# Optimization experiments

Hardware: AMD Instinct MI355X
Metric: run time of the kernel (lower is better)

## Reference

```python
import jax, jax.numpy as jnp
import numpy as np

N = 50000          # nodes
E = 800000         # directed edges (before self-loops)
NUM_CLASSES = 10
NEG_SLOPE = 0.2    # PyG GATConv default leaky_relu slope


def segment_softmax(logits, seg, num_segments):
    # numerically stable softmax over edges grouped by target node
    m = jax.ops.segment_max(logits, seg, num_segments=num_segments)
    e = jnp.exp(logits - m[seg])
    s = jax.ops.segment_sum(e, seg, num_segments=num_segments)
    return e / s[seg]


def gat_conv(x, src, dst, W, a_src, a_dst, b, n_nodes):
    # single-head PyG-style GATConv (eval mode: attention dropout disabled)
    h = x @ W                              # [N, C]
    alpha_src = h @ a_src                  # [N]
    alpha_dst = h @ a_dst                  # [N]
    logits = jax.nn.leaky_relu(alpha_src[src] + alpha_dst[dst], NEG_SLOPE)  # [E']
    alpha = segment_softmax(logits, dst, n_nodes)                            # [E']
    out = jax.ops.segment_sum(h[src] * alpha[:, None], dst, num_segments=n_nodes)
    return out + b


def setup_inputs() -> dict:
    key = jax.random.key(0)
    ks = jax.random.split(key, 13)
    x = jax.random.normal(ks[0], (N, 11), dtype=jnp.float32)
    edge_index = jax.random.randint(ks[1], (2, E), 0, N, dtype=jnp.int32)
    batch = jnp.zeros((N,), dtype=jnp.int32)  # unused by forward (no pooling)
    s = 0.1
    W1 = jax.random.normal(ks[2], (11, 16), jnp.float32) * s
    a1_src = jax.random.normal(ks[3], (16,), jnp.float32) * s
    a1_dst = jax.random.normal(ks[4], (16,), jnp.float32) * s
    b1 = jnp.zeros((16,), jnp.float32)
    W2 = jax.random.normal(ks[5], (16, 64), jnp.float32) * s
    a2_src = jax.random.normal(ks[6], (64,), jnp.float32) * s
    a2_dst = jax.random.normal(ks[7], (64,), jnp.float32) * s
    b2 = jnp.zeros((64,), jnp.float32)
    Wl = jax.random.normal(ks[8], (64, NUM_CLASSES), jnp.float32) * s
    bl = jnp.zeros((NUM_CLASSES,), jnp.float32)
    return {"x": x, "edge_index": edge_index, "batch": batch,
            "W1": W1, "a1_src": a1_src, "a1_dst": a1_dst, "b1": b1,
            "W2": W2, "a2_src": a2_src, "a2_dst": a2_dst, "b2": b2,
            "Wl": Wl, "bl": bl}


def reference(x, edge_index, batch, W1, a1_src, a1_dst, b1,
              W2, a2_src, a2_dst, b2, Wl, bl):
    n = x.shape[0]
    loop = jnp.arange(n, dtype=edge_index.dtype)
    src = jnp.concatenate([edge_index[0], loop])  # add self-loops (PyG default)
    dst = jnp.concatenate([edge_index[1], loop])
    h = gat_conv(x, src, dst, W1, a1_src, a1_dst, b1, n)
    h = jax.nn.relu(h)
    h = gat_conv(h, src, dst, W2, a2_src, a2_dst, b2, n)
    return h @ Wl + bl
```

## Files before the change

### kernel.cpp

```cpp
#include <hip/hip_runtime.h>
#include <hip/hip_bf16.h>
#include <hip/hip_fp16.h>

#define NEG_SLOPE 0.2f
#define BUCK 128
#define BSTRIDE 4096
#define SRCM 0x1FFFFFFu

__device__ __forceinline__ float lrelu(float x) {
    return x > 0.f ? x : NEG_SLOPE * x;
}

__global__ __launch_bounds__(256)
void front_kernel(const float* __restrict__ x,
                  const float* __restrict__ W1,
                  const float* __restrict__ a1s, const float* __restrict__ a1d,
                  __half* __restrict__ h, float* __restrict__ as, float* __restrict__ ad,
                  int n, int tb,
                  const float* __restrict__ W2,
                  const float* __restrict__ a2s, const float* __restrict__ a2d,
                  const float* __restrict__ b2,
                  const float* __restrict__ Wl, const float* __restrict__ bl,
                  float* __restrict__ va, float* __restrict__ vd,
                  float* __restrict__ Wc, float* __restrict__ bc,
                  int* __restrict__ gcur, int nbuck) {
    const int bid = blockIdx.x;
    if (bid < tb) {
        constexpr int F_IN = 11, C_OUT = 16;
        __shared__ float sW[F_IN * C_OUT];
        __shared__ float sAs[C_OUT];
        __shared__ float sAd[C_OUT];
        for (int i = threadIdx.x; i < F_IN * C_OUT; i += 256) sW[i] = W1[i];
        if (threadIdx.x < C_OUT) { sAs[threadIdx.x] = a1s[threadIdx.x]; sAd[threadIdx.x] = a1d[threadIdx.x]; }
        __syncthreads();
        int i = bid * 256 + threadIdx.x;
        if (i >= n) return;
        float xin[F_IN];
#pragma unroll
        for (int f = 0; f < F_IN; ++f) xin[f] = x[(size_t)i * F_IN + f];
        float r[C_OUT];
        float s_acc = 0.f, d_acc = 0.f;
#pragma unroll
        for (int c = 0; c < C_OUT; ++c) {
            float acc = 0.f;
#pragma unroll
            for (int f = 0; f < F_IN; ++f) acc = fmaf(xin[f], sW[f * C_OUT + c], acc);
            r[c] = acc;
            s_acc = fmaf(acc, sAs[c], s_acc);
            d_acc = fmaf(acc, sAd[c], d_acc);
        }
        unsigned int u[8];
#pragma unroll
        for (int k = 0; k < 8; ++k) {
            __half2 hh = __floats2half2_rn(r[2 * k], r[2 * k + 1]);
            u[k] = *reinterpret_cast<unsigned int*>(&hh);
        }
        uint4* hp = reinterpret_cast<uint4*>(&h[(size_t)i * 16]);
        hp[0] = make_uint4(u[0], u[1], u[2], u[3]);
        hp[1] = make_uint4(u[4], u[5], u[6], u[7]);
        as[i] = s_acc;
        ad[i] = d_acc;
    } else {
        int t = threadIdx.x;
        for (int i = t; i < nbuck; i += 256) gcur[i] = i * BSTRIDE;
        if (t < 16) {
            float s = 0.f, s2 = 0.f;
            for (int c = 0; c < 64; ++c) {
                float w = W2[t * 64 + c];
                s = fmaf(w, a2s[c], s);
                s2 = fmaf(w, a2d[c], s2);
            }
            va[t] = s; vd[t] = s2;
        }
        int i = t - 64;
        if (i >= 0 && i < 160) {
            int f = i / 10, k = i % 10;
            float s = 0.f;
            for (int c = 0; c < 64; ++c) s = fmaf(W2[f * 64 + c], Wl[c * 10 + k], s);
            Wc[i] = s;
        }
        int k2 = t - 240;
        if (k2 >= 0 && k2 < 10) {
            float s = bl[k2];
            for (int c = 0; c < 64; ++c) s = fmaf(b2[c], Wl[c * 10 + k2], s);
            bc[k2] = s;
        }
    }
}

__global__ __launch_bounds__(256)
void scatter_kernel(const int* __restrict__ ei, int E, int n, int CH,
                    int* __restrict__ gcur, uint2* __restrict__ pk, int nbuck,
                    const float* __restrict__ as1, const float* __restrict__ ad1) {
    __shared__ int lhist[512];
    for (int i = threadIdx.x; i < nbuck; i += 256) lhist[i] = 0;
    __syncthreads();
    const int beg = blockIdx.x * CH;
    const int end = min(beg + CH, E + n);
    for (int e = beg + threadIdx.x * 4; e < end; e += 1024) {
        if (e + 3 < E) {
            const int4 d4 = *reinterpret_cast<const int4*>(&ei[E + e]);
            atomicAdd(&lhist[d4.x >> 7], 1);
            atomicAdd(&lhist[d4.y >> 7], 1);
            atomicAdd(&lhist[d4.z >> 7], 1);
            atomicAdd(&lhist[d4.w >> 7], 1);
        } else {
            for (int k = 0; k < 4 && e + k < end; ++k) {
                int ee = e + k;
                int d = (ee < E) ? ei[E + ee] : (ee - E);
                atomicAdd(&lhist[d >> 7], 1);
            }
        }
    }
    __syncthreads();
    for (int i = threadIdx.x; i < nbuck; i += 256) {
        int c = lhist[i];
        lhist[i] = (c > 0) ? atomicAdd(&gcur[i], c) : 0;
    }
    __syncthreads();
    for (int e = beg + threadIdx.x * 4; e < end; e += 1024) {
        if (e + 3 < E) {
            const int4 s4 = *reinterpret_cast<const int4*>(&ei[e]);
            const int4 d4 = *reinterpret_cast<const int4*>(&ei[E + e]);
            float w0 = __expf(lrelu(as1[s4.x] + ad1[d4.x]));
            float w1 = __expf(lrelu(as1[s4.y] + ad1[d4.y]));
            float w2 = __expf(lrelu(as1[s4.z] + ad1[d4.z]));
            float w3 = __expf(lrelu(as1[s4.w] + ad1[d4.w]));
            int slot;
            slot = atomicAdd(&lhist[d4.x >> 7], 1);
            pk[slot] = make_uint2(((unsigned int)(d4.x & 127) << 25) | (unsigned int)s4.x, __float_as_uint(w0));
            slot = atomicAdd(&lhist[d4.y >> 7], 1);
            pk[slot] = make_uint2(((unsigned int)(d4.y & 127) << 25) | (unsigned int)s4.y, __float_as_uint(w1));
            slot = atomicAdd(&lhist[d4.z >> 7], 1);
            pk[slot] = make_uint2(((unsigned int)(d4.z & 127) << 25) | (unsigned int)s4.z, __float_as_uint(w2));
            slot = atomicAdd(&lhist[d4.w >> 7], 1);
            pk[slot] = make_uint2(((unsigned int)(d4.w & 127) << 25) | (unsigned int)s4.w, __float_as_uint(w3));
        } else {
            for (int k = 0; k < 4 && e + k < end; ++k) {
                int ee = e + k;
                int s, d;
                if (ee < E) { s = ei[ee]; d = ei[E + ee]; } else { s = d = ee - E; }
                float w = __expf(lrelu(as1[s] + ad1[d]));
                int slot = atomicAdd(&lhist[d >> 7], 1);
                pk[slot] = make_uint2(((unsigned int)(d & 127) << 25) | (unsigned int)s, __float_as_uint(w));
            }
        }
    }
}

__global__ __launch_bounds__(256)
void bucketsort_kernel(const uint2* __restrict__ pk,
                       const int* __restrict__ gcur,
                       uint2* __restrict__ cw,
                       int* __restrict__ row_beg, int* __restrict__ deg,
                       int n) {
    __shared__ int lcnt[BUCK];
    __shared__ int lofs[BUCK];
    const int tid = threadIdx.x;
    const int base = blockIdx.x * BUCK;
    const int beg = blockIdx.x * BSTRIDE;
    const int end = gcur[blockIdx.x];

    if (tid < BUCK) lcnt[tid] = 0;
    __syncthreads();
    for (int i = beg + tid * 2; i < end; i += 512) {
        if (i + 1 < end) {
            const uint4 q = *reinterpret_cast<const uint4*>(&pk[i]);
            atomicAdd(&lcnt[q.x >> 25], 1);
            atomicAdd(&lcnt[q.z >> 25], 1);
        } else {
            atomicAdd(&lcnt[pk[i].x >> 25], 1);
        }
    }
    __syncthreads();
    int v = 0;
    if (tid < BUCK) { v = lcnt[tid]; lofs[tid] = v; }
    __syncthreads();
    for (int off = 1; off < BUCK; off <<= 1) {
        int u = 0;
        if (tid < BUCK && tid >= off) u = lofs[tid - off];
        __syncthreads();
        if (tid < BUCK && tid >= off) lofs[tid] += u;
        __syncthreads();
    }
    if (tid < BUCK) {
        int excl = lofs[tid] - v;
        if (base + tid < n) {
            row_beg[base + tid] = beg + excl;
            deg[base + tid] = v;
        }
        lcnt[tid] = excl;
    }
    __syncthreads();
    for (int i = beg + tid * 2; i < end; i += 512) {
        if (i + 1 < end) {
            const uint4 q = *reinterpret_cast<const uint4*>(&pk[i]);
            int slot;
            slot = beg + atomicAdd(&lcnt[q.x >> 25], 1); cw[slot] = make_uint2(q.x, q.y);
            slot = beg + atomicAdd(&lcnt[q.z >> 25], 1); cw[slot] = make_uint2(q.z, q.w);
        } else {
            const uint2 q = pk[i];
            int slot = beg + atomicAdd(&lcnt[q.x >> 25], 1);
            cw[slot] = q;
        }
    }
}

__global__ void gat_agg1_kernel(const int* __restrict__ row_beg,
                                const int* __restrict__ deg,
                                const uint2* __restrict__ cw,
                                const __half* __restrict__ h,
                                const float* __restrict__ b1,
                                const float* __restrict__ va,
                                const float* __restrict__ vd,
                                __half* __restrict__ X1r,
                                float* __restrict__ as2,
                                float* __restrict__ ad2, int n) {
    __shared__ float sb1[16], sva[16], svd[16];
    if (threadIdx.x < 16) {
        sb1[threadIdx.x] = b1[threadIdx.x];
        sva[threadIdx.x] = va[threadIdx.x];
        svd[threadIdx.x] = vd[threadIdx.x];
    }
    __syncthreads();
    int node = (blockIdx.x * blockDim.x + threadIdx.x) >> 4;
    int sl = threadIdx.x & 15;
    if (node >= n) return;
    int beg = row_beg[node];
    int end = beg + deg[node];

    const int eq = sl >> 2;
    const int cl = sl & 3;
    float lsum = 0.f;
    float4 acc = {0.f, 0.f, 0.f, 0.f};
    for (int chunk = beg; chunk < end; chunk += 16) {
        int e = chunk + sl;
        float wv = 0.f; int sv = 0;
        if (e < end) {
            uint2 rec = cw[e];
            sv = (int)(rec.x & SRCM);
            wv = __uint_as_float(rec.y);
            lsum += wv;
        }
        const int nch = min(16, end - chunk);
        const int T = (nch + 3) >> 2;
        for (int t = 0; t < T; ++t) {
            int j = t * 4 + eq;
            float wj = __shfl(wv, j, 16);
            int   sj = __shfl(sv, j, 16);
            if (j < nch) {
                uint2 hv2 = *reinterpret_cast<const uint2*>(&h[(size_t)sj * 16 + cl * 4]);
                float2 f01 = __half22float2(*reinterpret_cast<__half2*>(&hv2.x));
                float2 f23 = __half22float2(*reinterpret_cast<__half2*>(&hv2.y));
                acc.x = fmaf(wj, f01.x, acc.x);
                acc.y = fmaf(wj, f01.y, acc.y);
                acc.z = fmaf(wj, f23.x, acc.z);
                acc.w = fmaf(wj, f23.y, acc.w);
            }
        }
    }
#pragma unroll
    for (int k = 1; k < 16; k <<= 1) lsum += __shfl_xor(lsum, k, 16);
#pragma unroll
    for (int k = 4; k < 16; k <<= 1) {
        acc.x += __shfl_xor(acc.x, k, 16);
        acc.y += __shfl_xor(acc.y, k, 16);
        acc.z += __shfl_xor(acc.z, k, 16);
        acc.w += __shfl_xor(acc.w, k, 16);
    }
    float inv = 1.f / lsum;
    float x0 = fmaxf(fmaf(acc.x, inv, sb1[cl * 4 + 0]), 0.f);
    float x1 = fmaxf(fmaf(acc.y, inv, sb1[cl * 4 + 1]), 0.f);
    float x2 = fmaxf(fmaf(acc.z, inv, sb1[cl * 4 + 2]), 0.f);
    float x3 = fmaxf(fmaf(acc.w, inv, sb1[cl * 4 + 3]), 0.f);
    if (eq == 0) {
        __half2 p01 = __floats2half2_rn(x0, x1);
        __half2 p23 = __floats2half2_rn(x2, x3);
        uint2 o = make_uint2(*reinterpret_cast<unsigned int*>(&p01),
                             *reinterpret_cast<unsigned int*>(&p23));
        *reinterpret_cast<uint2*>(&X1r[(size_t)node * 16 + cl * 4]) = o;
    }
    float p = x0 * sva[cl * 4] + x1 * sva[cl * 4 + 1] + x2 * sva[cl * 4 + 2] + x3 * sva[cl * 4 + 3];
    float q = x0 * svd[cl * 4] + x1 * svd[cl * 4 + 1] + x2 * svd[cl * 4 + 2] + x3 * svd[cl * 4 + 3];
    p += __shfl_xor(p, 1, 16); p += __shfl_xor(p, 2, 16);
    q += __shfl_xor(q, 1, 16); q += __shfl_xor(q, 2, 16);
    if (sl == 0) { as2[node] = p; ad2[node] = q; }
}

__global__ void gat_agg2_kernel(const int* __restrict__ row_beg,
                                const int* __restrict__ deg,
                                const uint2* __restrict__ cw,
                                const float* __restrict__ as2,
                                const float* __restrict__ ad2,
                                const __half* __restrict__ X1r,
                                const float* __restrict__ Wc,
                                const float* __restrict__ bc,
                                float* __restrict__ out, int n) {
    __shared__ float sWc[160], sbc[10];
    for (int i = threadIdx.x; i < 160; i += blockDim.x) sWc[i] = Wc[i];
    if (threadIdx.x < 10) sbc[threadIdx.x] = bc[threadIdx.x];
    __syncthreads();
    int node = (blockIdx.x * blockDim.x + threadIdx.x) >> 4;
    int sl = threadIdx.x & 15;
    if (node >= n) return;
    int beg = row_beg[node];
    int end = beg + deg[node];
    float add = ad2[node];

    const int eq = sl >> 2;
    const int cl = sl & 3;
    float lsum = 0.f;
    float4 acc = {0.f, 0.f, 0.f, 0.f};
    for (int chunk = beg; chunk < end; chunk += 16) {
        int e = chunk + sl;
        float wv = 0.f; int sv = 0;
        if (e < end) {
            sv = (int)(cw[e].x & SRCM);
            wv = __expf(lrelu(as2[sv] + add));
            lsum += wv;
        }
        const int nch = min(16, end - chunk);
        const int T = (nch + 3) >> 2;
        for (int t = 0; t < T; ++t) {
            int j = t * 4 + eq;
            float wj = __shfl(wv, j, 16);
            int   sj = __shfl(sv, j, 16);
            if (j < nch) {
                uint2 hv2 = *reinterpret_cast<const uint2*>(&X1r[(size_t)sj * 16 + cl * 4]);
                float2 f01 = __half22float2(*reinterpret_cast<__half2*>(&hv2.x));
                float2 f23 = __half22float2(*reinterpret_cast<__half2*>(&hv2.y));
                acc.x = fmaf(wj, f01.x, acc.x);
                acc.y = fmaf(wj, f01.y, acc.y);
                acc.z = fmaf(wj, f23.x, acc.z);
                acc.w = fmaf(wj, f23.y, acc.w);
            }
        }
    }
#pragma unroll
    for (int k = 1; k < 16; k <<= 1) lsum += __shfl_xor(lsum, k, 16);
#pragma unroll
    for (int k = 4; k < 16; k <<= 1) {
        acc.x += __shfl_xor(acc.x, k, 16);
        acc.y += __shfl_xor(acc.y, k, 16);
        acc.z += __shfl_xor(acc.z, k, 16);
        acc.w += __shfl_xor(acc.w, k, 16);
    }
    float inv = 1.f / lsum;
    acc.x *= inv; acc.y *= inv; acc.z *= inv; acc.w *= inv;
    float p[10];
#pragma unroll
    for (int k = 0; k < 10; ++k) {
        p[k] = acc.x * sWc[(cl * 4 + 0) * 10 + k]
             + acc.y * sWc[(cl * 4 + 1) * 10 + k]
             + acc.z * sWc[(cl * 4 + 2) * 10 + k]
             + acc.w * sWc[(cl * 4 + 3) * 10 + k];
    }
#pragma unroll
    for (int k = 0; k < 10; ++k) {
        p[k] += __shfl_xor(p[k], 1, 16);
        p[k] += __shfl_xor(p[k], 2, 16);
    }
    if (sl < 10) {
        float v = p[0];
#pragma unroll
        for (int k = 1; k < 10; ++k) v = (sl == k) ? p[k] : v;
        out[(size_t)node * 10 + sl] = v + sbc[sl];
    }
}

extern "C" void kernel_launch(void* const* d_in, const int* in_sizes, int n_in,
                              void* d_out, int out_size, void* d_ws, size_t ws_size,
                              hipStream_t stream) {
    const float* x       = (const float*)d_in[0];
    const int*   ei      = (const int*)d_in[1];
    const float* W1      = (const float*)d_in[3];
    const float* a1_src  = (const float*)d_in[4];
    const float* a1_dst  = (const float*)d_in[5];
    const float* b1      = (const float*)d_in[6];
    const float* W2      = (const float*)d_in[7];
    const float* a2_src  = (const float*)d_in[8];
    const float* a2_dst  = (const float*)d_in[9];
    const float* b2      = (const float*)d_in[10];
    const float* Wl      = (const float*)d_in[11];
    const float* bl      = (const float*)d_in[12];
    float* out = (float*)d_out;

    const int N = in_sizes[2];
    const int E = in_sizes[1] / 2;
    const int ET = E + N;

    const int B = 256;
    auto cdiv = [](int a, int b) { return (a + b - 1) / b; };

    const int NBUCK = cdiv(N, BUCK);
    const int NBLK  = 512;
    const int CHB   = ((cdiv(ET, NBLK) + 3) / 4) * 4;
    const int TB    = cdiv(N, B);

    char* ws = (char*)d_ws;
    size_t off = 0;
    auto alloc = [&](size_t bytes) {
        char* p = ws + off;
        off = (off + bytes + 255) & ~(size_t)255;
        return p;
    };
    __half*       h1   = (__half*)alloc((size_t)N * 16 * 2);
    __half*       X1r  = (__half*)alloc((size_t)N * 16 * 2);
    float*        as1  = (float*)alloc((size_t)N * 4);
    float*        ad1  = (float*)alloc((size_t)N * 4);
    float*        as2  = (float*)alloc((size_t)N * 4);
    float*        ad2  = (float*)alloc((size_t)N * 4);
    int*          rowb = (int*)alloc((size_t)N * 4);
    int*          degb = (int*)alloc((size_t)N * 4);
    uint2*        cw   = (uint2*)alloc((size_t)NBUCK * BSTRIDE * 8);
    uint2*        pk   = (uint2*)alloc((size_t)NBUCK * BSTRIDE * 8);
    int*          gcur = (int*)alloc((size_t)NBUCK * 4);
    float*        va   = (float*)alloc(16 * 4);
    float*        vd   = (float*)alloc(16 * 4);
    float*        Wc   = (float*)alloc(160 * 4);
    float*        bc   = (float*)alloc(10 * 4);
    (void)ws_size;

    front_kernel<<<TB + 1, B, 0, stream>>>(
        x, W1, a1_src, a1_dst, h1, as1, ad1, N, TB,
        W2, a2_src, a2_dst, b2, Wl, bl, va, vd, Wc, bc, gcur, NBUCK);

    scatter_kernel<<<NBLK, B, 0, stream>>>(ei, E, N, CHB, gcur, pk, NBUCK, as1, ad1);

    bucketsort_kernel<<<NBUCK, 256, 0, stream>>>(pk, gcur, cw, rowb, degb, N);

    gat_agg1_kernel<<<cdiv(N * 16, B), B, 0, stream>>>(rowb, degb, cw, h1, b1, va, vd, X1r, as2, ad2, N);

    gat_agg2_kernel<<<cdiv(N * 16, B), B, 0, stream>>>(rowb, degb, cw, as2, ad2, X1r, Wc, bc, out, N);
}
```

Baseline: 70.78 us.

## Register-cache scatter edges in fixed chunks and stage bucket sort through LDS

```diff
diff --git a/kernel.cpp b/kernel.cpp
--- a/kernel.cpp
+++ b/kernel.cpp
@@ -6,6 +6,7 @@
 #define BUCK 128
 #define BSTRIDE 4096
 #define SRCM 0x1FFFFFFu
+#define SCH 2048
 
 __device__ __forceinline__ float lrelu(float x) {
     return x > 0.f ? x : NEG_SLOPE * x;
@@ -89,63 +90,76 @@
 }
 
 __global__ __launch_bounds__(256)
-void scatter_kernel(const int* __restrict__ ei, int E, int n, int CH,
+void scatter_kernel(const int* __restrict__ ei, int E, int ET,
                     int* __restrict__ gcur, uint2* __restrict__ pk, int nbuck,
                     const float* __restrict__ as1, const float* __restrict__ ad1) {
     __shared__ int lhist[512];
     for (int i = threadIdx.x; i < nbuck; i += 256) lhist[i] = 0;
     __syncthreads();
-    const int beg = blockIdx.x * CH;
-    const int end = min(beg + CH, E + n);
-    for (int e = beg + threadIdx.x * 4; e < end; e += 1024) {
-        if (e + 3 < E) {
-            const int4 d4 = *reinterpret_cast<const int4*>(&ei[E + e]);
-            atomicAdd(&lhist[d4.x >> 7], 1);
-            atomicAdd(&lhist[d4.y >> 7], 1);
-            atomicAdd(&lhist[d4.z >> 7], 1);
-            atomicAdd(&lhist[d4.w >> 7], 1);
-        } else {
-            for (int k = 0; k < 4 && e + k < end; ++k) {
-                int ee = e + k;
-                int d = (ee < E) ? ei[E + ee] : (ee - E);
-                atomicAdd(&lhist[d >> 7], 1);
-            }
-        }
-    }
-    __syncthreads();
+    const int tid = threadIdx.x;
+    const int beg = blockIdx.x * SCH;
+
+    int rs0, rs1, rs2, rs3, rs4, rs5, rs6, rs7;
+    int rd0, rd1, rd2, rd3, rd4, rd5, rd6, rd7;
+    const int e0 = beg + tid * 4;
+    const int e1 = e0 + 1024;
+    if (e0 + 3 < E) {
+        const int4 s4 = *reinterpret_cast<const int4*>(&ei[e0]);
+        const int4 d4 = *reinterpret_cast<const int4*>(&ei[E + e0]);
+        rs0 = s4.x; rs1 = s4.y; rs2 = s4.z; rs3 = s4.w;
+        rd0 = d4.x; rd1 = d4.y; rd2 = d4.z; rd3 = d4.w;
+    } else {
+        rs0 = rd0 = (e0 + 0 < ET) ? ((e0 + 0 < E) ? 0 : e0 + 0 - E) : -1;
+        if (e0 + 0 < E) { rs0 = ei[e0 + 0]; rd0 = ei[E + e0 + 0]; }
+        rs1 = rd1 = (e0 + 1 < ET) ? ((e0 + 1 < E) ? 0 : e0 + 1 - E) : -1;
+        if (e0 + 1 < E) { rs1 = ei[e0 + 1]; rd1 = ei[E + e0 + 1]; }
+        rs2 = rd2 = (e0 + 2 < ET) ? ((e0 + 2 < E) ? 0 : e0 + 2 - E) : -1;
+        if (e0 + 2 < E) { rs2 = ei[e0 + 2]; rd2 = ei[E + e0 + 2]; }
+        rs3 = rd3 = (e0 + 3 < ET) ? ((e0 + 3 < E) ? 0 : e0 + 3 - E) : -1;
+        if (e0 + 3 < E) { rs3 = ei[e0 + 3]; rd3 = ei[E + e0 + 3]; }
+    }
+    if (e1 + 3 < E) {
+        const int4 s4 = *reinterpret_cast<const int4*>(&ei[e1]);
+        const int4 d4 = *reinterpret_cast<const int4*>(&ei[E + e1]);
+        rs4 = s4.x; rs5 = s4.y; rs6 = s4.z; rs7 = s4.w;
+        rd4 = d4.x; rd5 = d4.y; rd6 = d4.z; rd7 = d4.w;
+    } else {
+        rs4 = rd4 = (e1 + 0 < ET) ? ((e1 + 0 < E) ? 0 : e1 + 0 - E) : -1;
+        if (e1 + 0 < E) { rs4 = ei[e1 + 0]; rd4 = ei[E + e1 + 0]; }
+        rs5 = rd5 = (e1 + 1 < ET) ? ((e1 + 1 < E) ? 0 : e1 + 1 - E) : -1;
+        if (e1 + 1 < E) { rs5 = ei[e1 + 1]; rd5 = ei[E + e1 + 1]; }
+        rs6 = rd6 = (e1 + 2 < ET) ? ((e1 + 2 < E) ? 0 : e1 + 2 - E) : -1;
+        if (e1 + 2 < E) { rs6 = ei[e1 + 2]; rd6 = ei[E + e1 + 2]; }
+        rs7 = rd7 = (e1 + 3 < ET) ? ((e1 + 3 < E) ? 0 : e1 + 3 - E) : -1;
+        if (e1 + 3 < E) { rs7 = ei[e1 + 3]; rd7 = ei[E + e1 + 3]; }
+    }
+
+    if (rd0 >= 0) atomicAdd(&lhist[rd0 >> 7], 1);
+    if (rd1 >= 0) atomicAdd(&lhist[rd1 >> 7], 1);
+    if (rd2 >= 0) atomicAdd(&lhist[rd2 >> 7], 1);
+    if (rd3 >= 0) atomicAdd(&lhist[rd3 >> 7], 1);
+    if (rd4 >= 0) atomicAdd(&lhist[rd4 >> 7], 1);
+    if (rd5 >= 0) atomicAdd(&lhist[rd5 >> 7], 1);
+    if (rd6 >= 0) atomicAdd(&lhist[rd6 >> 7], 1);
+    if (rd7 >= 0) atomicAdd(&lhist[rd7 >> 7], 1);
+    __syncthreads();
+
     for (int i = threadIdx.x; i < nbuck; i += 256) {
         int c = lhist[i];
         lhist[i] = (c > 0) ? atomicAdd(&gcur[i], c) : 0;
     }
     __syncthreads();
-    for (int e = beg + threadIdx.x * 4; e < end; e += 1024) {
-        if (e + 3 < E) {
-            const int4 s4 = *reinterpret_cast<const int4*>(&ei[e]);
-            const int4 d4 = *reinterpret_cast<const int4*>(&ei[E + e]);
-            float w0 = __expf(lrelu(as1[s4.x] + ad1[d4.x]));
-            float w1 = __expf(lrelu(as1[s4.y] + ad1[d4.y]));
-            float w2 = __expf(lrelu(as1[s4.z] + ad1[d4.z]));
-            float w3 = __expf(lrelu(as1[s4.w] + ad1[d4.w]));
-            int slot;
-            slot = atomicAdd(&lhist[d4.x >> 7], 1);
-            pk[slot] = make_uint2(((unsigned int)(d4.x & 127) << 25) | (unsigned int)s4.x, __float_as_uint(w0));
-            slot = atomicAdd(&lhist[d4.y >> 7], 1);
-            pk[slot] = make_uint2(((unsigned int)(d4.y & 127) << 25) | (unsigned int)s4.y, __float_as_uint(w1));
-            slot = atomicAdd(&lhist[d4.z >> 7], 1);
-            pk[slot] = make_uint2(((unsigned int)(d4.z & 127) << 25) | (unsigned int)s4.z, __float_as_uint(w2));
-            slot = atomicAdd(&lhist[d4.w >> 7], 1);
-            pk[slot] = make_uint2(((unsigned int)(d4.w & 127) << 25) | (unsigned int)s4.w, __float_as_uint(w3));
-        } else {
-            for (int k = 0; k < 4 && e + k < end; ++k) {
-                int ee = e + k;
-                int s, d;
-                if (ee < E) { s = ei[ee]; d = ei[E + ee]; } else { s = d = ee - E; }
-                float w = __expf(lrelu(as1[s] + ad1[d]));
-                int slot = atomicAdd(&lhist[d >> 7], 1);
-                pk[slot] = make_uint2(((unsigned int)(d & 127) << 25) | (unsigned int)s, __float_as_uint(w));
-            }
-        }
-    }
+
+#define EMIT(RS, RD)                                                                   \
+    if (RD >= 0) {                                                                     \
+        float w = __expf(lrelu(as1[RS] + ad1[RD]));                                    \
+        int slot = atomicAdd(&lhist[RD >> 7], 1);                                      \
+        pk[slot] = make_uint2(((unsigned int)(RD & 127) << 25) | (unsigned int)RS,     \
+                              __float_as_uint(w));                                     \
+    }
+    EMIT(rs0, rd0) EMIT(rs1, rd1) EMIT(rs2, rd2) EMIT(rs3, rd3)
+    EMIT(rs4, rd4) EMIT(rs5, rd5) EMIT(rs6, rd6) EMIT(rs7, rd7)
+#undef EMIT
 }
 
 __global__ __launch_bounds__(256)
@@ -154,24 +168,26 @@
                        uint2* __restrict__ cw,
                        int* __restrict__ row_beg, int* __restrict__ deg,
                        int n) {
+    __shared__ uint2 sbuf[BSTRIDE];
+    __shared__ uint2 dbuf[BSTRIDE];
     __shared__ int lcnt[BUCK];
     __shared__ int lofs[BUCK];
     const int tid = threadIdx.x;
     const int base = blockIdx.x * BUCK;
     const int beg = blockIdx.x * BSTRIDE;
-    const int end = gcur[blockIdx.x];
+    const int cnt = gcur[blockIdx.x] - beg;
 
     if (tid < BUCK) lcnt[tid] = 0;
-    __syncthreads();
-    for (int i = beg + tid * 2; i < end; i += 512) {
-        if (i + 1 < end) {
-            const uint4 q = *reinterpret_cast<const uint4*>(&pk[i]);
-            atomicAdd(&lcnt[q.x >> 25], 1);
-            atomicAdd(&lcnt[q.z >> 25], 1);
+    for (int i = tid * 2; i < cnt; i += 512) {
+        if (i + 1 < cnt) {
+            *reinterpret_cast<uint4*>(&sbuf[i]) = *reinterpret_cast<const uint4*>(&pk[beg + i]);
         } else {
-            atomicAdd(&lcnt[pk[i].x >> 25], 1);
-        }
-    }
+            sbuf[i] = pk[beg + i];
+        }
+    }
+    __syncthreads();
+    for (int i = tid; i < cnt; i += 256)
+        atomicAdd(&lcnt[sbuf[i].x >> 25], 1);
     __syncthreads();
     int v = 0;
     if (tid < BUCK) { v = lcnt[tid]; lofs[tid] = v; }
@@ -192,16 +208,17 @@
         lcnt[tid] = excl;
     }
     __syncthreads();
-    for (int i = beg + tid * 2; i < end; i += 512) {
-        if (i + 1 < end) {
-            const uint4 q = *reinterpret_cast<const uint4*>(&pk[i]);
-            int slot;
-            slot = beg + atomicAdd(&lcnt[q.x >> 25], 1); cw[slot] = make_uint2(q.x, q.y);
-            slot = beg + atomicAdd(&lcnt[q.z >> 25], 1); cw[slot] = make_uint2(q.z, q.w);
+    for (int i = tid; i < cnt; i += 256) {
+        uint2 rec = sbuf[i];
+        int slot = atomicAdd(&lcnt[rec.x >> 25], 1);
+        dbuf[slot] = rec;
+    }
+    __syncthreads();
+    for (int i = tid * 2; i < cnt; i += 512) {
+        if (i + 1 < cnt) {
+            *reinterpret_cast<uint4*>(&cw[beg + i]) = *reinterpret_cast<uint4*>(&dbuf[i]);
         } else {
-            const uint2 q = pk[i];
-            int slot = beg + atomicAdd(&lcnt[q.x >> 25], 1);
-            cw[slot] = q;
+            cw[beg + i] = dbuf[i];
         }
     }
 }
@@ -393,8 +410,7 @@
     auto cdiv = [](int a, int b) { return (a + b - 1) / b; };
 
     const int NBUCK = cdiv(N, BUCK);
-    const int NBLK  = 512;
-    const int CHB   = ((cdiv(ET, NBLK) + 3) / 4) * 4;
+    const int NBLK  = cdiv(ET, SCH);
     const int TB    = cdiv(N, B);
 
     char* ws = (char*)d_ws;
@@ -425,7 +441,7 @@
         x, W1, a1_src, a1_dst, h1, as1, ad1, N, TB,
         W2, a2_src, a2_dst, b2, Wl, bl, va, vd, Wc, bc, gcur, NBUCK);
 
-    scatter_kernel<<<NBLK, B, 0, stream>>>(ei, E, N, CHB, gcur, pk, NBUCK, as1, ad1);
+    scatter_kernel<<<NBLK, B, 0, stream>>>(ei, E, ET, gcur, pk, NBUCK, as1, ad1);
 
     bucketsort_kernel<<<NBUCK, 256, 0, stream>>>(pk, gcur, cw, rowb, degb, N);
 
```

Measured after the change: 67.59 us. 1.05x faster.
